# Performance work log

Measured on AMD Instinct MI355X. Metric: run time of the kernel, lower is better.

Reference implementation:

```python
import jax, jax.numpy as jnp
import numpy as np

N, IN_FEAT, OUT_FEAT, H = 4096, 256, 256, 8
D = OUT_FEAT // H  # per-head dim = 32
ADJ_DENSITY = 0.05


def setup_inputs() -> dict:
    key = jax.random.key(0)
    kx, kw, kb, ka, kadj = jax.random.split(key, 5)
    x = jax.random.normal(kx, (N, IN_FEAT), dtype=jnp.float32)
    # eqx.nn.Linear params: weight [out, in], bias [out]
    W = jax.random.normal(kw, (OUT_FEAT, IN_FEAT), dtype=jnp.float32) * (1.0 / np.sqrt(IN_FEAT))
    b = jax.random.normal(kb, (OUT_FEAT,), dtype=jnp.float32) * 0.01
    a = jax.random.normal(ka, (H, 2 * D), dtype=jnp.float32)
    adj_matrix = jax.random.bernoulli(kadj, ADJ_DENSITY, (N, N)).astype(jnp.float32)
    return {"x": x, "W": W, "b": b, "a": a, "adj_matrix": adj_matrix}


def reference(x, W, b, a, adj_matrix):
    num_nodes = x.shape[0]
    num_heads = a.shape[0]
    half = a.shape[1] // 2
    # projection: [N, H*D] -> [N, H, D]
    node_feats = (x @ W.T + b).reshape(num_nodes, num_heads, half)
    # per-head additive attention halves -> [N, H]
    logit_parent = (node_feats * a[None, :, :half]).sum(axis=-1)
    logit_child = (node_feats * a[None, :, half:]).sum(axis=-1)
    # [N, N, H] dense logits via broadcast-add
    attn_logits = logit_parent[:, None, :] + logit_child[None, :, :]
    attn_logits = jax.nn.leaky_relu(attn_logits, 0.2)
    # NOTE: faithful to source — masked entries set to 0.0 (not -inf)
    attn_logits = jnp.where(jnp.abs(adj_matrix)[..., None] != 0.0, attn_logits, 0.0)
    attn_probs = jax.nn.softmax(attn_logits, axis=1)
    out = jnp.einsum('ijh,jhc->ihc', attn_probs, node_feats)
    return out.reshape(num_nodes, -1)
```

## Files before the change

### kernel.cpp

```cpp
#include <hip/hip_runtime.h>

#define NN    4096
#define OF    256
#define NH    8
#define MAXNZ 384

typedef __attribute__((ext_vector_type(8))) short short8;
typedef __attribute__((ext_vector_type(4))) float f32x4;

__device__ __forceinline__ float bf2f(unsigned int u) {
    union { unsigned int i; float f; } v; v.i = u << 16; return v.f;
}
__device__ __forceinline__ unsigned short f2bf(float f) {
    union { float f; unsigned int i; } v; v.f = f;
    unsigned int x = v.i;
    return (unsigned short)((x + 0x7fffu + ((x >> 16) & 1u)) >> 16);
}
__device__ __forceinline__ unsigned int pk2bf(float a, float b) {
    return (unsigned int)f2bf(a) | ((unsigned int)f2bf(b) << 16);
}

__global__ __launch_bounds__(256) void k_pre(
    const float* __restrict__ adjf, const float* __restrict__ Wf,
    int* __restrict__ flag, unsigned short* __restrict__ Wbh,
    unsigned short* __restrict__ Wbl, float* __restrict__ zbase)
{
    __shared__ int viol;
    int t = threadIdx.x;
    int gid = blockIdx.x * 256 + t;
    if (t == 0) viol = 0;
    __syncthreads();
    int bad = 0;
    for (int k = t; k < NN; k += 256) {
        float v = adjf[k];
        if (!(v == 0.0f || v == 1.0f)) bad = 1;
    }
    if (bad) atomicAdd(&viol, 1);
    __syncthreads();
    int f = viol > 0;
    if (t == 0) *flag = f;

    zbase[gid] = 0.f;
    if (gid < 256) zbase[65536 + gid] = 0.f;
    if (!f) {
        float v = Wf[gid];
        unsigned short h = f2bf(v);
        Wbh[gid] = h; Wbl[gid] = f2bf(v - bf2f(h));
    }
}

__global__ __launch_bounds__(256) void k_main(
    const void* __restrict__ xraw, const void* __restrict__ Wraw,
    const void* __restrict__ braw, const void* __restrict__ araw,
    const float* __restrict__ adjf, const int* __restrict__ flag,
    const unsigned short* __restrict__ Wbh, const unsigned short* __restrict__ Wbl,
    unsigned short* __restrict__ nfb, float* __restrict__ lp,
    float* __restrict__ lc, float* __restrict__ Stot,
    unsigned short* __restrict__ csr, int* __restrict__ nnz)
{
    __shared__ unsigned short xh[16][264], xl[16][264];
    __shared__ int wtot[4];

    int f = *flag;
    int t = threadIdx.x;
    int wave = t >> 6;
    int lane = t & 63;
    int bid = blockIdx.x;
    int bdiv3 = bid / 3;

    if (bid - bdiv3*3 == 0) {
        int tid  = bdiv3 * 4 + wave;
        int mt = tid >> 4, nt = tid & 15;
        int lr = lane & 15;
        int kq = (lane >> 4) * 8;

        if (!f) {
            const float* xsrc = (const float*)xraw + (size_t)mt * 4096;
            #pragma unroll
            for (int q = 0; q < 16; q++) {
                int e = t + 256*q;
                float v = xsrc[e];
                unsigned short h = f2bf(v);
                xh[e >> 8][e & 255] = h;
                xl[e >> 8][e & 255] = f2bf(v - bf2f(h));
            }
            __syncthreads();
        }

        size_t wo = (size_t)(nt*16 + lr)*OF + kq;
        f32x4 acc = {0.f, 0.f, 0.f, 0.f};
        if (f) {
            const short8* xp = reinterpret_cast<const short8*>(
                (const unsigned short*)xraw + (size_t)(mt*16 + lr)*OF + kq);
            const short8* wp = reinterpret_cast<const short8*>(
                (const unsigned short*)Wraw + wo);
            #pragma unroll
            for (int kk = 0; kk < OF/32; kk++)
                acc = __builtin_amdgcn_mfma_f32_16x16x32_bf16(xp[kk*4], wp[kk*4], acc, 0, 0, 0);
        } else {
            const short8* wh = reinterpret_cast<const short8*>(Wbh + wo);
            const short8* wl = reinterpret_cast<const short8*>(Wbl + wo);
            #pragma unroll
            for (int kk = 0; kk < OF/32; kk++) {
                short8 ah = *reinterpret_cast<const short8*>(&xh[lr][kk*32 + kq]);
                short8 al = *reinterpret_cast<const short8*>(&xl[lr][kk*32 + kq]);
                short8 bh = wh[kk*4], bl = wl[kk*4];
                acc = __builtin_amdgcn_mfma_f32_16x16x32_bf16(ah, bh, acc, 0, 0, 0);
                acc = __builtin_amdgcn_mfma_f32_16x16x32_bf16(ah, bl, acc, 0, 0, 0);
                acc = __builtin_amdgcn_mfma_f32_16x16x32_bf16(al, bh, acc, 0, 0, 0);
            }
        }

        int col  = nt*16 + lr;
        int row0 = mt*16 + (lane >> 4) * 4;
        int h = col >> 5, cc = col & 31;
        float bias, apar, achd;
        if (f) {
            bias = bf2f((unsigned int)((const unsigned short*)braw)[col]);
            apar = bf2f((unsigned int)((const unsigned short*)araw)[h*64 + cc]);
            achd = bf2f((unsigned int)((const unsigned short*)araw)[h*64 + 32 + cc]);
        } else {
            bias = ((const float*)braw)[col];
            apar = ((const float*)araw)[h*64 + cc];
            achd = ((const float*)araw)[h*64 + 32 + cc];
        }
        float st = 0.f, pr[4], cr[4];
        #pragma unroll
        for (int r = 0; r < 4; r++) {
            float v = acc[r] + bias;
            nfb[(size_t)(row0 + r) * OF + col] = f2bf(v);
            st += v;
            pr[r] = v * apar;
            cr[r] = v * achd;
        }
        #pragma unroll
        for (int m = 1; m <= 8; m <<= 1) {
            #pragma unroll
            for (int r = 0; r < 4; r++) {
                pr[r] += __shfl_xor(pr[r], m, 64);
                cr[r] += __shfl_xor(cr[r], m, 64);
            }
        }
        if ((lane & 15) == 0) {
            #pragma unroll
            for (int r = 0; r < 4; r++) {
                atomicAdd(&lp[(row0 + r) * NH + h], pr[r]);
                atomicAdd(&lc[(row0 + r) * NH + h], cr[r]);
            }
        }
        st += __shfl_down(st, 16, 64);
        st += __shfl_down(st, 32, 64);
        if (lane < 16) atomicAdd(&Stot[col], st);
    } else {
        int sid = bid - bdiv3 - 1;
        int r    = sid*2 + (wave >> 1);
        int half = wave & 1;

        unsigned int m32 = 0;
        if (f) {
            const uint4* ap = reinterpret_cast<const uint4*>(
                (const unsigned short*)adjf + (size_t)r * NN + half * 2048);
            #pragma unroll
            for (int g = 0; g < 4; g++) {
                uint4 v = ap[lane + 64*g];
                unsigned int wd[4] = {v.x, v.y, v.z, v.w};
                #pragma unroll
                for (int u = 0; u < 4; u++) {
                    if (wd[u] & 0xffffu) m32 |= 1u << (g*8 + 2*u);
                    if (wd[u] >> 16)     m32 |= 1u << (g*8 + 2*u + 1);
                }
            }
        } else {
            const uint4* ap = reinterpret_cast<const uint4*>(
                adjf + (size_t)r * NN + half * 2048);
            #pragma unroll
            for (int g = 0; g < 8; g++) {
                uint4 v = ap[lane + 64*g];
                if (v.x) m32 |= 1u << (g*4);
                if (v.y) m32 |= 1u << (g*4 + 1);
                if (v.z) m32 |= 1u << (g*4 + 2);
                if (v.w) m32 |= 1u << (g*4 + 3);
            }
        }

        int pc = __popc(m32);
        int pref = pc;
        #pragma unroll
        for (int off = 1; off < 64; off <<= 1) {
            int u = __shfl_up(pref, off, 64);
            if (lane >= off) pref += u;
        }
        if (lane == 63) wtot[wave] = pref;
        __syncthreads();
        int base = (wave == 1) ? wtot[0] : (wave == 3) ? wtot[2] : 0;
        if (lane == 0) {
            if (wave == 0) nnz[r] = min(wtot[0] + wtot[1], MAXNZ);
            if (wave == 2) nnz[r] = min(wtot[2] + wtot[3], MAXNZ);
        }
        int pos = base + pref - pc;
        unsigned int mm = m32;
        int jb = half * 2048;
        while (mm && pos < MAXNZ) {
            int q = __builtin_ctz(mm);
            mm &= mm - 1;
            int j = f ? (jb + lane*8 + ((q >> 3) << 9) + (q & 7))
                      : (jb + lane*4 + ((q >> 2) << 8) + (q & 3));
            csr[(size_t)r * MAXNZ + pos++] = (unsigned short)j;
        }
    }
}

__global__ __launch_bounds__(256, 8) void k_attn(
    const int* __restrict__ flag, const unsigned short* __restrict__ csr,
    const int* __restrict__ nnz,
    const float* __restrict__ lp, const float* __restrict__ lc,
    const unsigned short* __restrict__ nfb, const float* __restrict__ Stot,
    void* __restrict__ outv)
{
    __shared__ float lps[NH];
    __shared__ int   jro[MAXNZ];
    __shared__ float wlist[MAXNZ][NH];
    __shared__ float zred[256];
    __shared__ float gred[3][256];

    int i = blockIdx.x;
    int t = threadIdx.x;
    int lane = t & 63, wid = t >> 6;
    int f = *flag;
    if (t < NH) lps[t] = lp[i*NH + t];
    int n = min(nnz[i], MAXNZ);

    if (t < MAXNZ/8) {
        uint4 v = reinterpret_cast<const uint4*>(csr + (size_t)i * MAXNZ)[t];
        unsigned int ws[4] = {v.x, v.y, v.z, v.w};
        #pragma unroll
        for (int u = 0; u < 4; u++) {
            jro[t*8 + 2*u]     = (int)(ws[u] & 0xffffu) * OF;
            jro[t*8 + 2*u + 1] = (int)(ws[u] >> 16) * OF;
        }
    }
    __syncthreads();

    int h8 = t & 7, c32 = t >> 3;
    float lph = lps[h8];
    float zp = 0.f;
    int k3 = c32;
    for (; k3 + 32 < n; k3 += 64) {
        int j0 = jro[k3] >> 5, j1 = jro[k3 + 32] >> 5;
        float l0 = lc[j0 + h8], l1 = lc[j1 + h8];
        float s0 = lph + l0; s0 = s0 > 0.f ? s0 : 0.2f * s0;
        float s1 = lph + l1; s1 = s1 > 0.f ? s1 : 0.2f * s1;
        float w0 = __expf(fminf(s0, 70.f)) - 1.f;
        float w1 = __expf(fminf(s1, 70.f)) - 1.f;
        wlist[k3][h8] = w0; wlist[k3 + 32][h8] = w1;
        zp += w0 + w1;
    }
    if (k3 < n) {
        float s = lph + lc[(jro[k3] >> 5) + h8];
        s = s > 0.f ? s : 0.2f * s;
        float w = __expf(fminf(s, 70.f)) - 1.f;
        wlist[k3][h8] = w;
        zp += w;
    }
    zred[t] = zp;
    __syncthreads();

    int hh = lane >> 3;
    int c4 = lane * 4;
    float a0 = 0.f, a1 = 0.f, a2 = 0.f, a3 = 0.f;
    int k = wid;
    for (; k + 28 < n; k += 32) {
        int jj[8]; float ww[8];
        #pragma unroll
        for (int u = 0; u < 8; u++) {
            jj[u] = __builtin_amdgcn_readfirstlane(jro[k + 4*u]);
            ww[u] = wlist[k + 4*u][hh];
        }
        uint2 d[8];
        #pragma unroll
        for (int u = 0; u < 8; u++)
            d[u] = *reinterpret_cast<const uint2*>(nfb + jj[u] + c4);
        #pragma unroll
        for (int u = 0; u < 8; u++) {
            a0 += ww[u] * bf2f(d[u].x & 0xffffu);
            a1 += ww[u] * bf2f(d[u].x >> 16);
            a2 += ww[u] * bf2f(d[u].y & 0xffffu);
            a3 += ww[u] * bf2f(d[u].y >> 16);
        }
    }
    for (; k < n; k += 4) {
        int j = __builtin_amdgcn_readfirstlane(jro[k]);
        float w = wlist[k][hh];
        uint2 d = *reinterpret_cast<const uint2*>(nfb + j + c4);
        a0 += w * bf2f(d.x & 0xffffu);
        a1 += w * bf2f(d.x >> 16);
        a2 += w * bf2f(d.y & 0xffffu);
        a3 += w * bf2f(d.y >> 16);
    }
    if (wid) {
        gred[wid-1][c4]   = a0; gred[wid-1][c4+1] = a1;
        gred[wid-1][c4+2] = a2; gred[wid-1][c4+3] = a3;
    }
    __syncthreads();

    if (wid == 0) {
        float z = zred[lane] + zred[lane+64] + zred[lane+128] + zred[lane+192];
        z += __shfl_down(z, 32, 64);
        z += __shfl_down(z, 16, 64);
        z += __shfl_down(z, 8, 64);
        float zfull = __shfl(z, hh, 64);
        float iz = 1.0f / (4096.0f + zfull);
        a0 += gred[0][c4]   + gred[1][c4]   + gred[2][c4];
        a1 += gred[0][c4+1] + gred[1][c4+1] + gred[2][c4+1];
        a2 += gred[0][c4+2] + gred[1][c4+2] + gred[2][c4+2];
        a3 += gred[0][c4+3] + gred[1][c4+3] + gred[2][c4+3];
        float4 stv = *reinterpret_cast<const float4*>(Stot + c4);
        float o0 = (stv.x + a0) * iz;
        float o1 = (stv.y + a1) * iz;
        float o2 = (stv.z + a2) * iz;
        float o3 = (stv.w + a3) * iz;
        if (f) {
            uint2 pk; pk.x = pk2bf(o0, o1); pk.y = pk2bf(o2, o3);
            *reinterpret_cast<uint2*>((unsigned short*)outv + (size_t)i*OF + c4) = pk;
        } else {
            float4 o = {o0, o1, o2, o3};
            *reinterpret_cast<float4*>((float*)outv + (size_t)i*OF + c4) = o;
        }
    }
}

extern "C" void kernel_launch(void* const* d_in, const int* in_sizes, int n_in,
                              void* d_out, int out_size, void* d_ws, size_t ws_size,
                              hipStream_t stream) {
    const void* x   = d_in[0];
    const void* W   = d_in[1];
    const void* b   = d_in[2];
    const void* a   = d_in[3];
    const void* adj = d_in[4];

    char* ws = (char*)d_ws;
    const size_t MB = 1024u*1024u, KB = 1024u;
    unsigned short* nfb  = (unsigned short*)(ws);
    float*          lp   = (float*)(ws + 2*MB);
    float*          lc   = (float*)(ws + 2*MB + 128*KB);
    float*          Stot = (float*)(ws + 2*MB + 256*KB);
    int*            flag = (int*)(ws + 2*MB + 257*KB);
    unsigned short* csr  = (unsigned short*)(ws + 2*MB + 258*KB);
    int*            nnz  = (int*)(ws + 5*MB + 258*KB);
    unsigned short* Wbh  = (unsigned short*)(ws + 6*MB);
    unsigned short* Wbl  = (unsigned short*)(ws + 6*MB + 128*KB);

    k_pre  <<<256,  256, 0, stream>>>((const float*)adj, (const float*)W,
                                      flag, Wbh, Wbl, lp);
    k_main <<<3072, 256, 0, stream>>>(x, W, b, a, (const float*)adj, flag,
                                      Wbh, Wbl, nfb, lp, lc, Stot, csr, nnz);
    k_attn <<<NN,   256, 0, stream>>>(flag, csr, nnz, lp, lc, nfb, Stot, d_out);
}
```

Measured before the change: 154.5 us.

## Build adjacency neighbor list inside attention kernel instead of a separate CSR pass

The adjacency-scan-to-CSR work moves out of the combined projection/scan kernel and into the attention kernel. Each attention block now scans its own adjacency row, prefix-sums the set bits across four waves, and writes neighbor offsets straight into shared memory. This removes the global CSR and nnz buffers and their write/read round trip, and the projection kernel shrinks to a 1024-block pure GEMM launch. In exchange, the adjacency scan now runs on the attention kernel's critical path and cannot overlap with the projection work as it did before.

```diff
diff --git a/kernel.cpp b/kernel.cpp
--- a/kernel.cpp
+++ b/kernel.cpp
@@ -49,170 +49,108 @@
     }
 }
 
-__global__ __launch_bounds__(256) void k_main(
+__global__ __launch_bounds__(256) void k_proj(
     const void* __restrict__ xraw, const void* __restrict__ Wraw,
     const void* __restrict__ braw, const void* __restrict__ araw,
-    const float* __restrict__ adjf, const int* __restrict__ flag,
+    const int* __restrict__ flag,
     const unsigned short* __restrict__ Wbh, const unsigned short* __restrict__ Wbl,
     unsigned short* __restrict__ nfb, float* __restrict__ lp,
-    float* __restrict__ lc, float* __restrict__ Stot,
-    unsigned short* __restrict__ csr, int* __restrict__ nnz)
+    float* __restrict__ lc, float* __restrict__ Stot)
 {
     __shared__ unsigned short xh[16][264], xl[16][264];
-    __shared__ int wtot[4];
 
     int f = *flag;
     int t = threadIdx.x;
     int wave = t >> 6;
     int lane = t & 63;
-    int bid = blockIdx.x;
-    int bdiv3 = bid / 3;
-
-    if (bid - bdiv3*3 == 0) {
-        int tid  = bdiv3 * 4 + wave;
-        int mt = tid >> 4, nt = tid & 15;
-        int lr = lane & 15;
-        int kq = (lane >> 4) * 8;
-
-        if (!f) {
-            const float* xsrc = (const float*)xraw + (size_t)mt * 4096;
-            #pragma unroll
-            for (int q = 0; q < 16; q++) {
-                int e = t + 256*q;
-                float v = xsrc[e];
-                unsigned short h = f2bf(v);
-                xh[e >> 8][e & 255] = h;
-                xl[e >> 8][e & 255] = f2bf(v - bf2f(h));
-            }
-            __syncthreads();
-        }
-
-        size_t wo = (size_t)(nt*16 + lr)*OF + kq;
-        f32x4 acc = {0.f, 0.f, 0.f, 0.f};
-        if (f) {
-            const short8* xp = reinterpret_cast<const short8*>(
-                (const unsigned short*)xraw + (size_t)(mt*16 + lr)*OF + kq);
-            const short8* wp = reinterpret_cast<const short8*>(
-                (const unsigned short*)Wraw + wo);
-            #pragma unroll
-            for (int kk = 0; kk < OF/32; kk++)
-                acc = __builtin_amdgcn_mfma_f32_16x16x32_bf16(xp[kk*4], wp[kk*4], acc, 0, 0, 0);
-        } else {
-            const short8* wh = reinterpret_cast<const short8*>(Wbh + wo);
-            const short8* wl = reinterpret_cast<const short8*>(Wbl + wo);
-            #pragma unroll
-            for (int kk = 0; kk < OF/32; kk++) {
-                short8 ah = *reinterpret_cast<const short8*>(&xh[lr][kk*32 + kq]);
-                short8 al = *reinterpret_cast<const short8*>(&xl[lr][kk*32 + kq]);
-                short8 bh = wh[kk*4], bl = wl[kk*4];
-                acc = __builtin_amdgcn_mfma_f32_16x16x32_bf16(ah, bh, acc, 0, 0, 0);
-                acc = __builtin_amdgcn_mfma_f32_16x16x32_bf16(ah, bl, acc, 0, 0, 0);
-                acc = __builtin_amdgcn_mfma_f32_16x16x32_bf16(al, bh, acc, 0, 0, 0);
-            }
-        }
-
-        int col  = nt*16 + lr;
-        int row0 = mt*16 + (lane >> 4) * 4;
-        int h = col >> 5, cc = col & 31;
-        float bias, apar, achd;
-        if (f) {
-            bias = bf2f((unsigned int)((const unsigned short*)braw)[col]);
-            apar = bf2f((unsigned int)((const unsigned short*)araw)[h*64 + cc]);
-            achd = bf2f((unsigned int)((const unsigned short*)araw)[h*64 + 32 + cc]);
-        } else {
-            bias = ((const float*)braw)[col];
-            apar = ((const float*)araw)[h*64 + cc];
-            achd = ((const float*)araw)[h*64 + 32 + cc];
-        }
-        float st = 0.f, pr[4], cr[4];
+    int pid = blockIdx.x;
+
+    int tid  = pid * 4 + wave;
+    int mt = tid >> 4, nt = tid & 15;
+    int lr = lane & 15;
+    int kq = (lane >> 4) * 8;
+
+    if (!f) {
+        const float* xsrc = (const float*)xraw + (size_t)mt * 4096;
+        #pragma unroll
+        for (int q = 0; q < 16; q++) {
+            int e = t + 256*q;
+            float v = xsrc[e];
+            unsigned short h = f2bf(v);
+            xh[e >> 8][e & 255] = h;
+            xl[e >> 8][e & 255] = f2bf(v - bf2f(h));
+        }
+        __syncthreads();
+    }
+
+    size_t wo = (size_t)(nt*16 + lr)*OF + kq;
+    f32x4 acc = {0.f, 0.f, 0.f, 0.f};
+    if (f) {
+        const short8* xp = reinterpret_cast<const short8*>(
+            (const unsigned short*)xraw + (size_t)(mt*16 + lr)*OF + kq);
+        const short8* wp = reinterpret_cast<const short8*>(
+            (const unsigned short*)Wraw + wo);
+        #pragma unroll
+        for (int kk = 0; kk < OF/32; kk++)
+            acc = __builtin_amdgcn_mfma_f32_16x16x32_bf16(xp[kk*4], wp[kk*4], acc, 0, 0, 0);
+    } else {
+        const short8* wh = reinterpret_cast<const short8*>(Wbh + wo);
+        const short8* wl = reinterpret_cast<const short8*>(Wbl + wo);
+        #pragma unroll
+        for (int kk = 0; kk < OF/32; kk++) {
+            short8 ah = *reinterpret_cast<const short8*>(&xh[lr][kk*32 + kq]);
+            short8 al = *reinterpret_cast<const short8*>(&xl[lr][kk*32 + kq]);
+            short8 bh = wh[kk*4], bl = wl[kk*4];
+            acc = __builtin_amdgcn_mfma_f32_16x16x32_bf16(ah, bh, acc, 0, 0, 0);
+            acc = __builtin_amdgcn_mfma_f32_16x16x32_bf16(ah, bl, acc, 0, 0, 0);
+            acc = __builtin_amdgcn_mfma_f32_16x16x32_bf16(al, bh, acc, 0, 0, 0);
+        }
+    }
+
+    int col  = nt*16 + lr;
+    int row0 = mt*16 + (lane >> 4) * 4;
+    int h = col >> 5, cc = col & 31;
+    float bias, apar, achd;
+    if (f) {
+        bias = bf2f((unsigned int)((const unsigned short*)braw)[col]);
+        apar = bf2f((unsigned int)((const unsigned short*)araw)[h*64 + cc]);
+        achd = bf2f((unsigned int)((const unsigned short*)araw)[h*64 + 32 + cc]);
+    } else {
+        bias = ((const float*)braw)[col];
+        apar = ((const float*)araw)[h*64 + cc];
+        achd = ((const float*)araw)[h*64 + 32 + cc];
+    }
+    float st = 0.f, pr[4], cr[4];
+    #pragma unroll
+    for (int r = 0; r < 4; r++) {
+        float v = acc[r] + bias;
+        nfb[(size_t)(row0 + r) * OF + col] = f2bf(v);
+        st += v;
+        pr[r] = v * apar;
+        cr[r] = v * achd;
+    }
+    #pragma unroll
+    for (int m = 1; m <= 8; m <<= 1) {
         #pragma unroll
         for (int r = 0; r < 4; r++) {
-            float v = acc[r] + bias;
-            nfb[(size_t)(row0 + r) * OF + col] = f2bf(v);
-            st += v;
-            pr[r] = v * apar;
-            cr[r] = v * achd;
-        }
-        #pragma unroll
-        for (int m = 1; m <= 8; m <<= 1) {
-            #pragma unroll
-            for (int r = 0; r < 4; r++) {
-                pr[r] += __shfl_xor(pr[r], m, 64);
-                cr[r] += __shfl_xor(cr[r], m, 64);
-            }
-        }
-        if ((lane & 15) == 0) {
-            #pragma unroll
-            for (int r = 0; r < 4; r++) {
-                atomicAdd(&lp[(row0 + r) * NH + h], pr[r]);
-                atomicAdd(&lc[(row0 + r) * NH + h], cr[r]);
-            }
-        }
-        st += __shfl_down(st, 16, 64);
-        st += __shfl_down(st, 32, 64);
-        if (lane < 16) atomicAdd(&Stot[col], st);
-    } else {
-        int sid = bid - bdiv3 - 1;
-        int r    = sid*2 + (wave >> 1);
-        int half = wave & 1;
-
-        unsigned int m32 = 0;
-        if (f) {
-            const uint4* ap = reinterpret_cast<const uint4*>(
-                (const unsigned short*)adjf + (size_t)r * NN + half * 2048);
-            #pragma unroll
-            for (int g = 0; g < 4; g++) {
-                uint4 v = ap[lane + 64*g];
-                unsigned int wd[4] = {v.x, v.y, v.z, v.w};
-                #pragma unroll
-                for (int u = 0; u < 4; u++) {
-                    if (wd[u] & 0xffffu) m32 |= 1u << (g*8 + 2*u);
-                    if (wd[u] >> 16)     m32 |= 1u << (g*8 + 2*u + 1);
-                }
-            }
-        } else {
-            const uint4* ap = reinterpret_cast<const uint4*>(
-                adjf + (size_t)r * NN + half * 2048);
-            #pragma unroll
-            for (int g = 0; g < 8; g++) {
-                uint4 v = ap[lane + 64*g];
-                if (v.x) m32 |= 1u << (g*4);
-                if (v.y) m32 |= 1u << (g*4 + 1);
-                if (v.z) m32 |= 1u << (g*4 + 2);
-                if (v.w) m32 |= 1u << (g*4 + 3);
-            }
-        }
-
-        int pc = __popc(m32);
-        int pref = pc;
-        #pragma unroll
-        for (int off = 1; off < 64; off <<= 1) {
-            int u = __shfl_up(pref, off, 64);
-            if (lane >= off) pref += u;
-        }
-        if (lane == 63) wtot[wave] = pref;
-        __syncthreads();
-        int base = (wave == 1) ? wtot[0] : (wave == 3) ? wtot[2] : 0;
-        if (lane == 0) {
-            if (wave == 0) nnz[r] = min(wtot[0] + wtot[1], MAXNZ);
-            if (wave == 2) nnz[r] = min(wtot[2] + wtot[3], MAXNZ);
-        }
-        int pos = base + pref - pc;
-        unsigned int mm = m32;
-        int jb = half * 2048;
-        while (mm && pos < MAXNZ) {
-            int q = __builtin_ctz(mm);
-            mm &= mm - 1;
-            int j = f ? (jb + lane*8 + ((q >> 3) << 9) + (q & 7))
-                      : (jb + lane*4 + ((q >> 2) << 8) + (q & 3));
-            csr[(size_t)r * MAXNZ + pos++] = (unsigned short)j;
-        }
-    }
+            pr[r] += __shfl_xor(pr[r], m, 64);
+            cr[r] += __shfl_xor(cr[r], m, 64);
+        }
+    }
+    if ((lane & 15) == 0) {
+        #pragma unroll
+        for (int r = 0; r < 4; r++) {
+            atomicAdd(&lp[(row0 + r) * NH + h], pr[r]);
+            atomicAdd(&lc[(row0 + r) * NH + h], cr[r]);
+        }
+    }
+    st += __shfl_down(st, 16, 64);
+    st += __shfl_down(st, 32, 64);
+    if (lane < 16) atomicAdd(&Stot[col], st);
 }
 
 __global__ __launch_bounds__(256, 8) void k_attn(
-    const int* __restrict__ flag, const unsigned short* __restrict__ csr,
-    const int* __restrict__ nnz,
+    const int* __restrict__ flag, const float* __restrict__ adjf,
     const float* __restrict__ lp, const float* __restrict__ lc,
     const unsigned short* __restrict__ nfb, const float* __restrict__ Stot,
     void* __restrict__ outv)
@@ -222,22 +160,62 @@
     __shared__ float wlist[MAXNZ][NH];
     __shared__ float zred[256];
     __shared__ float gred[3][256];
+    __shared__ int   wtot[4];
 
     int i = blockIdx.x;
     int t = threadIdx.x;
     int lane = t & 63, wid = t >> 6;
     int f = *flag;
     if (t < NH) lps[t] = lp[i*NH + t];
-    int n = min(nnz[i], MAXNZ);
-
-    if (t < MAXNZ/8) {
-        uint4 v = reinterpret_cast<const uint4*>(csr + (size_t)i * MAXNZ)[t];
-        unsigned int ws[4] = {v.x, v.y, v.z, v.w};
-        #pragma unroll
-        for (int u = 0; u < 4; u++) {
-            jro[t*8 + 2*u]     = (int)(ws[u] & 0xffffu) * OF;
-            jro[t*8 + 2*u + 1] = (int)(ws[u] >> 16) * OF;
-        }
+
+    unsigned int m16 = 0;
+    if (f) {
+        const uint4* ap = reinterpret_cast<const uint4*>(
+            (const unsigned short*)adjf + (size_t)i * NN + wid * 1024);
+        #pragma unroll
+        for (int g = 0; g < 2; g++) {
+            uint4 v = ap[lane + 64*g];
+            unsigned int wd[4] = {v.x, v.y, v.z, v.w};
+            #pragma unroll
+            for (int u = 0; u < 4; u++) {
+                if (wd[u] & 0xffffu) m16 |= 1u << (g*8 + 2*u);
+                if (wd[u] >> 16)     m16 |= 1u << (g*8 + 2*u + 1);
+            }
+        }
+    } else {
+        const uint4* ap = reinterpret_cast<const uint4*>(
+            adjf + (size_t)i * NN + wid * 1024);
+        #pragma unroll
+        for (int g = 0; g < 4; g++) {
+            uint4 v = ap[lane + 64*g];
+            if (v.x) m16 |= 1u << (g*4);
+            if (v.y) m16 |= 1u << (g*4 + 1);
+            if (v.z) m16 |= 1u << (g*4 + 2);
+            if (v.w) m16 |= 1u << (g*4 + 3);
+        }
+    }
+
+    int pc = __popc(m16);
+    int pref = pc;
+    #pragma unroll
+    for (int off = 1; off < 64; off <<= 1) {
+        int u = __shfl_up(pref, off, 64);
+        if (lane >= off) pref += u;
+    }
+    if (lane == 63) wtot[wid] = pref;
+    __syncthreads();
+    int w0 = wtot[0], w1 = wtot[1], w2 = wtot[2], w3 = wtot[3];
+    int n = min(w0 + w1 + w2 + w3, MAXNZ);
+    int base = (wid > 0 ? w0 : 0) + (wid > 1 ? w1 : 0) + (wid > 2 ? w2 : 0);
+    int pos = base + pref - pc;
+    unsigned int mm = m16;
+    int jb = wid * 1024;
+    while (mm && pos < MAXNZ) {
+        int q = __builtin_ctz(mm);
+        mm &= mm - 1;
+        int j = f ? (jb + lane*8 + ((q >> 3) << 9) + (q & 7))
+                  : (jb + lane*4 + ((q >> 2) << 8) + (q & 3));
+        jro[pos++] = j * OF;
     }
     __syncthreads();
 
@@ -345,14 +323,13 @@
     float*          lc   = (float*)(ws + 2*MB + 128*KB);
     float*          Stot = (float*)(ws + 2*MB + 256*KB);
     int*            flag = (int*)(ws + 2*MB + 257*KB);
-    unsigned short* csr  = (unsigned short*)(ws + 2*MB + 258*KB);
-    int*            nnz  = (int*)(ws + 5*MB + 258*KB);
     unsigned short* Wbh  = (unsigned short*)(ws + 6*MB);
     unsigned short* Wbl  = (unsigned short*)(ws + 6*MB + 128*KB);
 
     k_pre  <<<256,  256, 0, stream>>>((const float*)adj, (const float*)W,
                                       flag, Wbh, Wbl, lp);
-    k_main <<<3072, 256, 0, stream>>>(x, W, b, a, (const float*)adj, flag,
-                                      Wbh, Wbl, nfb, lp, lc, Stot, csr, nnz);
-    k_attn <<<NN,   256, 0, stream>>>(flag, csr, nnz, lp, lc, nfb, Stot, d_out);
-}
+    k_proj <<<1024, 256, 0, stream>>>(x, W, b, a, flag, Wbh, Wbl,
+                                      nfb, lp, lc, Stot);
+    k_attn <<<NN,   256, 0, stream>>>(flag, (const float*)adj, lp, lc,
+                                      nfb, Stot, d_out);
+}
```

Result: no change. 154.1 us (median of 2 runs) (-0.3%).
